# Performance work log

Hardware: AMD Instinct MI355X
Metric: run time of the kernel (lower is better)

Reference implementation:

```python
import jax, jax.numpy as jnp
import numpy as np
from jax import lax

B, C, H, W = 64, 256, 32, 32
EPS = 1e-5


def setup_inputs() -> dict:
    key = jax.random.key(0)
    ks = jax.random.split(key, 11)
    c = C
    return {
        "x": jax.random.normal(ks[0], (B, C, H, W), jnp.float32),
        "bn1_gamma": jax.random.uniform(ks[1], (c,), jnp.float32, 0.5, 1.5),
        "bn1_beta": 0.1 * jax.random.normal(ks[2], (c,), jnp.float32),
        "bn1_mean": 0.1 * jax.random.normal(ks[3], (c,), jnp.float32),
        "bn1_var": jax.random.uniform(ks[4], (c,), jnp.float32, 0.5, 1.5),
        "w1": 0.05 * jax.random.normal(ks[5], (c, c, 3, 3), jnp.float32),
        "bn2_gamma": jax.random.uniform(ks[6], (c,), jnp.float32, 0.5, 1.5),
        "bn2_beta": 0.1 * jax.random.normal(ks[7], (c,), jnp.float32),
        "bn2_mean": 0.1 * jax.random.normal(ks[8], (c,), jnp.float32),
        "bn2_var": jax.random.uniform(ks[9], (c,), jnp.float32, 0.5, 1.5),
        "w2": 0.05 * jax.random.normal(ks[10], (c, c, 3, 3), jnp.float32),
    }


def _bn(x, gamma, beta, mean, var):
    # eval-mode BatchNorm2d over channel axis of NCHW
    inv = gamma * lax.rsqrt(var + EPS)
    return x * inv[None, :, None, None] + (beta - mean * inv)[None, :, None, None]


def _binarize(x):
    # TBN binary activations {-1,+1}, straight-through in bwd
    s = jnp.where(x >= 0, 1.0, -1.0).astype(x.dtype)
    return x + lax.stop_gradient(s - x)


def _ternarize(w):
    # TBN ternary weights alpha*{-1,0,+1}; delta = 0.7*mean|W|
    aw = jnp.abs(w)
    delta = 0.7 * jnp.mean(aw)
    mask = (aw > delta).astype(w.dtype)
    alpha = jnp.sum(aw * mask) / jnp.maximum(jnp.sum(mask), 1.0)
    wq = alpha * jnp.sign(w) * mask
    return w + lax.stop_gradient(wq - w)


def _tbn_conv3x3(x, w, stride):
    return lax.conv_general_dilated(
        _binarize(x), _ternarize(w),
        window_strides=(stride, stride), padding=[(1, 1), (1, 1)],
        dimension_numbers=("NCHW", "OIHW", "NCHW"))


def reference(x, bn1_gamma, bn1_beta, bn1_mean, bn1_var, w1,
              bn2_gamma, bn2_beta, bn2_mean, bn2_var, w2):
    identity = x
    h = _tbn_conv3x3(_bn(x, bn1_gamma, bn1_beta, bn1_mean, bn1_var), w1, 1)
    h = _tbn_conv3x3(_bn(h, bn2_gamma, bn2_beta, bn2_mean, bn2_var), w2, 1)
    return identity + h  # ShortCut downsample
```

## Files before the change

### kernel.cpp

```cpp
#include <hip/hip_runtime.h>
#include <stdint.h>


#define EPS 1e-5f

typedef int i32x4  __attribute__((ext_vector_type(4)));
typedef int i32x16 __attribute__((ext_vector_type(16)));

__device__ __forceinline__ void gload16(const void* g, void* l) {
  __builtin_amdgcn_global_load_lds(
      (const __attribute__((address_space(1))) void*)g,
      (__attribute__((address_space(3))) void*)l, 16, 0, 0);
}

__global__ __launch_bounds__(256) void wsum_kernel(const float* __restrict__ w,
                                                   float* __restrict__ partial) {
  __shared__ float red[256];
  const int t = threadIdx.x;
  const int b = blockIdx.x;
  float s = 0.f;
#pragma unroll
  for (int i = 0; i < 32; ++i) s += fabsf(w[b * 256 + t + i * 18432]);
  red[t] = s;
  __syncthreads();
  for (int o = 128; o > 0; o >>= 1) {
    if (t < o) red[t] += red[t + o];
    __syncthreads();
  }
  if (t == 0) partial[b] = red[0];
}

__global__ void delta_kernel(const float* __restrict__ p1, const float* __restrict__ p2,
                             float* __restrict__ delta) {
  const int t = threadIdx.x;
  if (t < 2) {
    const float* p = (t == 0) ? p1 : p2;
    double s = 0.0;
    for (int i = 0; i < 72; ++i) s += (double)p[i];
    delta[t] = 0.7f * (float)(s * (1.0 / 589824.0));
  }
}

__global__ __launch_bounds__(256) void quant_kernel(const float* __restrict__ w,
                                                    const float* __restrict__ delta2, const int didx,
                                                    int8_t* __restrict__ wq,
                                                    float* __restrict__ psum,
                                                    float* __restrict__ pcnt) {
  __shared__ float rs[256];
  __shared__ float rc[256];
  const int t = threadIdx.x;
  const int idx = blockIdx.x * 256 + t;
  const float d = delta2[didx];
  const float v = w[idx];
  const float av = fabsf(v);
  const bool m = av > d;
  const int co = idx / 2304;
  const int rem = idx - co * 2304;
  const int ci = rem / 9;
  const int tap = rem - ci * 9;
  wq[(co >> 5) * 73728 + (ci >> 6) * 18432 + tap * 2048 +
     (((ci & 63) >> 4) << 9) + ((co & 31) << 4) + (ci & 15)] =
      m ? (v > 0.f ? (int8_t)1 : (int8_t)-1) : (int8_t)0;
  rs[t] = m ? av : 0.f;
  rc[t] = m ? 1.f : 0.f;
  __syncthreads();
  for (int o = 128; o > 0; o >>= 1) {
    if (t < o) { rs[t] += rs[t + o]; rc[t] += rc[t + o]; }
    __syncthreads();
  }
  if (t == 0) { psum[blockIdx.x] = rs[0]; pcnt[blockIdx.x] = rc[0]; }
}

__global__ __launch_bounds__(256) void alpha_kernel(const float* __restrict__ ps1, const float* __restrict__ pc1,
                                                    const float* __restrict__ ps2, const float* __restrict__ pc2,
                                                    const float* __restrict__ g2, const float* __restrict__ b2,
                                                    const float* __restrict__ m2, const float* __restrict__ v2,
                                                    float* __restrict__ alphas,
                                                    float* __restrict__ inv2o, float* __restrict__ add2o) {
  __shared__ float rs[256];
  __shared__ float rc[256];
  const int t = threadIdx.x;
  float s1 = 0.f, c1 = 0.f, s2 = 0.f, c2 = 0.f;
#pragma unroll
  for (int i = 0; i < 9; ++i) {
    s1 += ps1[t + (i << 8)]; c1 += pc1[t + (i << 8)];
    s2 += ps2[t + (i << 8)]; c2 += pc2[t + (i << 8)];
  }
  rs[t] = s1; rc[t] = c1;
  __syncthreads();
  for (int o = 128; o > 0; o >>= 1) {
    if (t < o) { rs[t] += rs[t + o]; rc[t] += rc[t + o]; }
    __syncthreads();
  }
  if (t == 0) alphas[0] = rs[0] / fmaxf(rc[0], 1.f);
  __syncthreads();
  rs[t] = s2; rc[t] = c2;
  __syncthreads();
  for (int o = 128; o > 0; o >>= 1) {
    if (t < o) { rs[t] += rs[t + o]; rc[t] += rc[t + o]; }
    __syncthreads();
  }
  if (t == 0) alphas[1] = rs[0] / fmaxf(rc[0], 1.f);
  const float inv = g2[t] * rsqrtf(v2[t] + EPS);
  inv2o[t] = inv;
  add2o[t] = b2[t] - m2[t] * inv;
}

__global__ __launch_bounds__(256) void bn_bin_kernel(const float* __restrict__ x,
                                                     const float* __restrict__ g1,
                                                     const float* __restrict__ b1,
                                                     const float* __restrict__ m1,
                                                     const float* __restrict__ v1,
                                                     int8_t* __restrict__ a1) {
  __shared__ int8_t lds[64 * 40];
  const int t = threadIdx.x;
  const int p0 = blockIdx.x << 6;
  const int c0 = blockIdx.y << 5;
  const int n = blockIdx.z;
  const int pl = t & 63;
  const int cl0 = t >> 6;
#pragma unroll
  for (int i = 0; i < 8; ++i) {
    const int cl = cl0 + (i << 2);
    const int c = c0 + cl;
    const float inv = g1[c] * rsqrtf(v1[c] + EPS);
    const float ad = b1[c] - m1[c] * inv;
    const float val = x[(((n << 8) + c) << 10) + p0 + pl];
    const float tt = fmaf(val, inv, ad);
    lds[pl * 40 + cl] = (tt >= 0.f) ? (int8_t)1 : (int8_t)-1;
  }
  __syncthreads();
  const int pl2 = t >> 2;
  const int s2 = (t & 3) << 3;
  const uint2 o = *(const uint2*)&lds[pl2 * 40 + s2];
  *(uint2*)&a1[(((n << 10) + p0 + pl2) << 8) + c0 + s2] = o;
}

template <int EPI>
__global__ __launch_bounds__(256, 4) void conv3x3_tbn(
    const int8_t* __restrict__ act,
    const int8_t* __restrict__ wq,
    const float* __restrict__ alphas, const int aidx,
    const float* __restrict__ inv2, const float* __restrict__ add2,
    const float* __restrict__ xres,
    int8_t* __restrict__ aout, float* __restrict__ fout) {
  __shared__ int8_t ldsA[4 * 321 * 16];
  __shared__ int8_t ldsB[9 * 4 * 32 * 16];

  const int tid = threadIdx.x;
  const int bid = blockIdx.x;
  const int L = (bid & 7) * 256 + (bid >> 3);
  const int mb = L >> 3;
  const int nb = L & 7;
  const int n = mb >> 2;
  const int y0 = (mb & 3) << 3;
  const int l = tid & 63;
  const int wid = tid >> 6;
  const int lx = l & 31;
  const int lh = l >> 5;

  int srcA[5], dstA[5];
#pragma unroll
  for (int i = 0; i < 5; ++i) {
    const int idx = tid + (i << 8);
    const int asl = idx / 320;
    const int apx = idx - asl * 320;
    int ys = y0 - 1 + (apx >> 5);
    ys = ys < 0 ? 0 : (ys > 31 ? 31 : ys);
    srcA[i] = (((n << 10) + (ys << 5) + (apx & 31)) << 8) + (asl << 4);
    dstA[i] = asl * 5136 + (apx << 4);
  }
  if (tid < 4) *(i32x4*)(ldsA + tid * 5136 + 5120) = (i32x4){0, 0, 0, 0};

  i32x16 acc[2];
  acc[0] = (i32x16)(0);
  acc[1] = (i32x16)(0);

  const int8_t* wbase = wq + nb * 73728;

#pragma unroll
  for (int i = 0; i < 5; ++i) gload16(act + srcA[i], ldsA + dstA[i]);
#pragma unroll
  for (int i = 0; i < 4; ++i)
    gload16(wbase + ((tid + (i << 8)) << 4), ldsB + ((tid + (i << 8)) << 4));
  if (tid < 128) gload16(wbase + ((tid + 1024) << 4), ldsB + ((tid + 1024) << 4));
  __syncthreads();

  for (int chunk = 0; chunk < 4; ++chunk) {
    __builtin_amdgcn_s_setprio(1);
#pragma unroll
    for (int tap = 0; tap < 9; ++tap) {
      const int ky = tap / 3, kx = tap % 3;
      const int xs = lx + kx - 1;
      const bool xok = (unsigned)xs < 32u;
      int apix[2];
#pragma unroll
      for (int mt = 0; mt < 2; ++mt) {
        const int yr = (wid << 1) + mt + ky;
        const bool ok = xok && ((unsigned)(y0 - 1 + yr) < 32u);
        apix[mt] = ok ? (yr << 5) + xs : 320;
      }
      i32x4 bfr[2], afr[2][2];
#pragma unroll
      for (int kh = 0; kh < 2; ++kh) {
        const int sl = lh + (kh << 1);
        bfr[kh] = *(const i32x4*)(ldsB + (tap << 11) + (sl << 9) + (lx << 4));
#pragma unroll
        for (int mt = 0; mt < 2; ++mt)
          afr[mt][kh] = *(const i32x4*)(ldsA + sl * 5136 + (apix[mt] << 4));
      }
#pragma unroll
      for (int mt = 0; mt < 2; ++mt)
#pragma unroll
        for (int kh = 0; kh < 2; ++kh)
          acc[mt] = __builtin_amdgcn_mfma_i32_32x32x32_i8(afr[mt][kh], bfr[kh], acc[mt], 0, 0, 0);
    }
    __builtin_amdgcn_s_setprio(0);
    if (chunk < 3) {
      __syncthreads();
#pragma unroll
      for (int i = 0; i < 5; ++i)
        gload16(act + srcA[i] + ((chunk + 1) << 6), ldsA + dstA[i]);
      const int8_t* wch = wbase + (chunk + 1) * 18432;
#pragma unroll
      for (int i = 0; i < 4; ++i)
        gload16(wch + ((tid + (i << 8)) << 4), ldsB + ((tid + (i << 8)) << 4));
      if (tid < 128) gload16(wch + ((tid + 1024) << 4), ldsB + ((tid + 1024) << 4));
      __syncthreads();
    }
  }

  const float alpha = alphas[aidx];
  const int co = (nb << 5) + lx;
  if constexpr (EPI == 0) {
    const float inv = inv2[co];
    const float ad = add2[co];
#pragma unroll
    for (int mt = 0; mt < 2; ++mt) {
      const int pixbase = (mb << 8) + (((wid << 1) + mt) << 5) + (lh << 2);
#pragma unroll
      for (int rg = 0; rg < 16; ++rg) {
        const int pix = pixbase + (rg & 3) + ((rg >> 2) << 3);
        const float h = alpha * (float)acc[mt][rg];
        const float tt = fmaf(h, inv, ad);
        aout[(pix << 8) + co] = (tt >= 0.f) ? (int8_t)1 : (int8_t)-1;
      }
    }
  } else {
#pragma unroll
    for (int mt = 0; mt < 2; ++mt) {
      const int pimg0 = ((mb & 3) << 8) + (((wid << 1) + mt) << 5) + (lh << 2);
#pragma unroll
      for (int qd = 0; qd < 4; ++qd) {
        const int off = (((n << 8) + co) << 10) + pimg0 + (qd << 3);
        const float4 xv = *(const float4*)(xres + off);
        float4 o;
        o.x = xv.x + alpha * (float)acc[mt][qd * 4 + 0];
        o.y = xv.y + alpha * (float)acc[mt][qd * 4 + 1];
        o.z = xv.z + alpha * (float)acc[mt][qd * 4 + 2];
        o.w = xv.w + alpha * (float)acc[mt][qd * 4 + 3];
        *(float4*)(fout + off) = o;
      }
    }
  }
}

extern "C" void kernel_launch(void* const* d_in, const int* in_sizes, int n_in,
                              void* d_out, int out_size, void* d_ws, size_t ws_size,
                              hipStream_t stream) {
  const float* x  = (const float*)d_in[0];
  const float* g1 = (const float*)d_in[1];
  const float* b1 = (const float*)d_in[2];
  const float* m1 = (const float*)d_in[3];
  const float* v1 = (const float*)d_in[4];
  const float* w1 = (const float*)d_in[5];
  const float* g2 = (const float*)d_in[6];
  const float* b2 = (const float*)d_in[7];
  const float* m2 = (const float*)d_in[8];
  const float* v2 = (const float*)d_in[9];
  const float* w2 = (const float*)d_in[10];
  float* out = (float*)d_out;

  char* ws = (char*)d_ws;
  int8_t* a1  = (int8_t*)(ws);
  int8_t* a2  = (int8_t*)(ws + 16777216);
  int8_t* wq1 = (int8_t*)(ws + 33554432);
  int8_t* wq2 = (int8_t*)(ws + 33554432 + 589824);
  float* fs = (float*)(ws + 33554432 + 1179648);
  float* pd1    = fs;
  float* pd2    = fs + 128;
  float* deltas = fs + 256;
  float* alphas = fs + 260;
  float* ps1    = fs + 512;
  float* pc1    = fs + 512 + 2304;
  float* ps2    = fs + 512 + 4608;
  float* pc2    = fs + 512 + 6912;
  float* inv2   = fs + 512 + 9216;
  float* add2   = fs + 512 + 9472;

  hipLaunchKernelGGL(wsum_kernel, dim3(72), dim3(256), 0, stream, w1, pd1);
  hipLaunchKernelGGL(wsum_kernel, dim3(72), dim3(256), 0, stream, w2, pd2);
  hipLaunchKernelGGL(delta_kernel, dim3(1), dim3(64), 0, stream, pd1, pd2, deltas);
  hipLaunchKernelGGL(quant_kernel, dim3(2304), dim3(256), 0, stream, w1, deltas, 0, wq1, ps1, pc1);
  hipLaunchKernelGGL(quant_kernel, dim3(2304), dim3(256), 0, stream, w2, deltas, 1, wq2, ps2, pc2);
  hipLaunchKernelGGL(alpha_kernel, dim3(1), dim3(256), 0, stream,
                     ps1, pc1, ps2, pc2, g2, b2, m2, v2, alphas, inv2, add2);
  hipLaunchKernelGGL(bn_bin_kernel, dim3(16, 8, 64), dim3(256), 0, stream, x, g1, b1, m1, v1, a1);
  hipLaunchKernelGGL((conv3x3_tbn<0>), dim3(2048), dim3(256), 0, stream,
                     a1, wq1, alphas, 0, inv2, add2, (const float*)nullptr,
                     a2, (float*)nullptr);
  hipLaunchKernelGGL((conv3x3_tbn<1>), dim3(2048), dim3(256), 0, stream,
                     a2, wq2, alphas, 1, (const float*)nullptr, (const float*)nullptr, x,
                     (int8_t*)nullptr, out);
  (void)in_sizes; (void)n_in; (void)out_size; (void)ws_size;
}
```

Baseline: 135.7 us.

## Enlarge conv tile to 16 rows x 64 channels with 512-thread blocks

The int8 MFMA conv kernel now uses 512-thread blocks. Each block covers 16 output rows by 64 output channels instead of 8 rows by 32 channels, and each wave holds a 2x2 grid of 32x32 accumulators. The weight quantization layout is changed to match 64-channel groups. This is meant to improve reuse of activation and weight fragments loaded from LDS and global memory, and to reduce halo overhead. In exchange it uses more LDS and registers per block and launches fewer blocks (512), which may reduce occupancy.

```diff
diff --git a/kernel.cpp b/kernel.cpp
--- a/kernel.cpp
+++ b/kernel.cpp
@@ -58,8 +58,8 @@
   const int rem = idx - co * 2304;
   const int ci = rem / 9;
   const int tap = rem - ci * 9;
-  wq[(co >> 5) * 73728 + (ci >> 6) * 18432 + tap * 2048 +
-     (((ci & 63) >> 4) << 9) + ((co & 31) << 4) + (ci & 15)] =
+  wq[(co >> 6) * 147456 + (ci >> 6) * 36864 + tap * 4096 +
+     (((ci & 63) >> 4) << 10) + ((co & 63) << 4) + (ci & 15)] =
       m ? (v > 0.f ? (int8_t)1 : (int8_t)-1) : (int8_t)0;
   rs[t] = m ? av : 0.f;
   rc[t] = m ? 1.f : 0.f;
@@ -137,53 +137,56 @@
 }
 
 template <int EPI>
-__global__ __launch_bounds__(256, 4) void conv3x3_tbn(
+__global__ __launch_bounds__(512, 4) void conv3x3_tbn(
     const int8_t* __restrict__ act,
     const int8_t* __restrict__ wq,
     const float* __restrict__ alphas, const int aidx,
     const float* __restrict__ inv2, const float* __restrict__ add2,
     const float* __restrict__ xres,
     int8_t* __restrict__ aout, float* __restrict__ fout) {
-  __shared__ int8_t ldsA[4 * 321 * 16];
-  __shared__ int8_t ldsB[9 * 4 * 32 * 16];
+  __shared__ int8_t ldsA[4 * 577 * 16];
+  __shared__ int8_t ldsB[9 * 4 * 64 * 16];
 
   const int tid = threadIdx.x;
   const int bid = blockIdx.x;
-  const int L = (bid & 7) * 256 + (bid >> 3);
-  const int mb = L >> 3;
-  const int nb = L & 7;
-  const int n = mb >> 2;
-  const int y0 = (mb & 3) << 3;
+  const int L = (bid & 7) * 64 + (bid >> 3);
+  const int mb = L >> 2;
+  const int nb = L & 3;
+  const int n = mb >> 1;
+  const int y0 = (mb & 1) << 4;
   const int l = tid & 63;
   const int wid = tid >> 6;
   const int lx = l & 31;
   const int lh = l >> 5;
 
-  int srcA[5], dstA[5];
+  int srcA[5];
 #pragma unroll
   for (int i = 0; i < 5; ++i) {
-    const int idx = tid + (i << 8);
-    const int asl = idx / 320;
-    const int apx = idx - asl * 320;
+    const int idx = tid + (i << 9);
+    const int asl = idx / 576;
+    const int apx = idx - asl * 576;
     int ys = y0 - 1 + (apx >> 5);
     ys = ys < 0 ? 0 : (ys > 31 ? 31 : ys);
     srcA[i] = (((n << 10) + (ys << 5) + (apx & 31)) << 8) + (asl << 4);
-    dstA[i] = asl * 5136 + (apx << 4);
-  }
-  if (tid < 4) *(i32x4*)(ldsA + tid * 5136 + 5120) = (i32x4){0, 0, 0, 0};
-
-  i32x16 acc[2];
-  acc[0] = (i32x16)(0);
-  acc[1] = (i32x16)(0);
-
-  const int8_t* wbase = wq + nb * 73728;
-
-#pragma unroll
-  for (int i = 0; i < 5; ++i) gload16(act + srcA[i], ldsA + dstA[i]);
-#pragma unroll
-  for (int i = 0; i < 4; ++i)
-    gload16(wbase + ((tid + (i << 8)) << 4), ldsB + ((tid + (i << 8)) << 4));
-  if (tid < 128) gload16(wbase + ((tid + 1024) << 4), ldsB + ((tid + 1024) << 4));
+  }
+  if (tid < 4) *(i32x4*)(ldsA + tid * 9232 + 9216) = (i32x4){0, 0, 0, 0};
+
+  i32x16 acc[2][2];
+  acc[0][0] = (i32x16)(0); acc[0][1] = (i32x16)(0);
+  acc[1][0] = (i32x16)(0); acc[1][1] = (i32x16)(0);
+
+  const int8_t* wbase = wq + nb * 147456;
+
+#pragma unroll
+  for (int i = 0; i < 5; ++i) {
+    const int idx = tid + (i << 9);
+    if (i < 4 || tid < 256) {
+      const int asl = idx / 576;
+      const int apx = idx - asl * 576;
+      gload16(act + srcA[i], ldsA + asl * 9232 + (apx << 4));
+      gload16(wbase + (idx << 4), ldsB + (idx << 4));
+    }
+  }
   __syncthreads();
 
   for (int chunk = 0; chunk < 4; ++chunk) {
@@ -198,68 +201,82 @@
       for (int mt = 0; mt < 2; ++mt) {
         const int yr = (wid << 1) + mt + ky;
         const bool ok = xok && ((unsigned)(y0 - 1 + yr) < 32u);
-        apix[mt] = ok ? (yr << 5) + xs : 320;
-      }
-      i32x4 bfr[2], afr[2][2];
+        apix[mt] = ok ? (yr << 5) + xs : 576;
+      }
+      i32x4 afr[2][2], bfr[2][2];
 #pragma unroll
       for (int kh = 0; kh < 2; ++kh) {
         const int sl = lh + (kh << 1);
-        bfr[kh] = *(const i32x4*)(ldsB + (tap << 11) + (sl << 9) + (lx << 4));
 #pragma unroll
         for (int mt = 0; mt < 2; ++mt)
-          afr[mt][kh] = *(const i32x4*)(ldsA + sl * 5136 + (apix[mt] << 4));
+          afr[mt][kh] = *(const i32x4*)(ldsA + sl * 9232 + (apix[mt] << 4));
+#pragma unroll
+        for (int nt = 0; nt < 2; ++nt)
+          bfr[nt][kh] = *(const i32x4*)(ldsB + (tap << 12) + (sl << 10) + ((nt << 5) + lx) * 16);
       }
 #pragma unroll
       for (int mt = 0; mt < 2; ++mt)
 #pragma unroll
-        for (int kh = 0; kh < 2; ++kh)
-          acc[mt] = __builtin_amdgcn_mfma_i32_32x32x32_i8(afr[mt][kh], bfr[kh], acc[mt], 0, 0, 0);
+        for (int nt = 0; nt < 2; ++nt)
+#pragma unroll
+          for (int kh = 0; kh < 2; ++kh)
+            acc[mt][nt] = __builtin_amdgcn_mfma_i32_32x32x32_i8(afr[mt][kh], bfr[nt][kh], acc[mt][nt], 0, 0, 0);
     }
     __builtin_amdgcn_s_setprio(0);
     if (chunk < 3) {
       __syncthreads();
-#pragma unroll
-      for (int i = 0; i < 5; ++i)
-        gload16(act + srcA[i] + ((chunk + 1) << 6), ldsA + dstA[i]);
-      const int8_t* wch = wbase + (chunk + 1) * 18432;
-#pragma unroll
-      for (int i = 0; i < 4; ++i)
-        gload16(wch + ((tid + (i << 8)) << 4), ldsB + ((tid + (i << 8)) << 4));
-      if (tid < 128) gload16(wch + ((tid + 1024) << 4), ldsB + ((tid + 1024) << 4));
+      const int8_t* wch = wbase + (chunk + 1) * 36864;
+#pragma unroll
+      for (int i = 0; i < 5; ++i) {
+        const int idx = tid + (i << 9);
+        if (i < 4 || tid < 256) {
+          const int asl = idx / 576;
+          const int apx = idx - asl * 576;
+          gload16(act + srcA[i] + ((chunk + 1) << 6), ldsA + asl * 9232 + (apx << 4));
+          gload16(wch + (idx << 4), ldsB + (idx << 4));
+        }
+      }
       __syncthreads();
     }
   }
 
   const float alpha = alphas[aidx];
-  const int co = (nb << 5) + lx;
   if constexpr (EPI == 0) {
-    const float inv = inv2[co];
-    const float ad = add2[co];
-#pragma unroll
-    for (int mt = 0; mt < 2; ++mt) {
-      const int pixbase = (mb << 8) + (((wid << 1) + mt) << 5) + (lh << 2);
-#pragma unroll
-      for (int rg = 0; rg < 16; ++rg) {
-        const int pix = pixbase + (rg & 3) + ((rg >> 2) << 3);
-        const float h = alpha * (float)acc[mt][rg];
-        const float tt = fmaf(h, inv, ad);
-        aout[(pix << 8) + co] = (tt >= 0.f) ? (int8_t)1 : (int8_t)-1;
+#pragma unroll
+    for (int nt = 0; nt < 2; ++nt) {
+      const int co = (nb << 6) + (nt << 5) + lx;
+      const float inv = inv2[co];
+      const float ad = add2[co];
+#pragma unroll
+      for (int mt = 0; mt < 2; ++mt) {
+        const int pixbase = (mb << 9) + (((wid << 1) + mt) << 5) + (lh << 2);
+#pragma unroll
+        for (int rg = 0; rg < 16; ++rg) {
+          const int pix = pixbase + (rg & 3) + ((rg >> 2) << 3);
+          const float h = alpha * (float)acc[mt][nt][rg];
+          const float tt = fmaf(h, inv, ad);
+          aout[(pix << 8) + co] = (tt >= 0.f) ? (int8_t)1 : (int8_t)-1;
+        }
       }
     }
   } else {
 #pragma unroll
-    for (int mt = 0; mt < 2; ++mt) {
-      const int pimg0 = ((mb & 3) << 8) + (((wid << 1) + mt) << 5) + (lh << 2);
-#pragma unroll
-      for (int qd = 0; qd < 4; ++qd) {
-        const int off = (((n << 8) + co) << 10) + pimg0 + (qd << 3);
-        const float4 xv = *(const float4*)(xres + off);
-        float4 o;
-        o.x = xv.x + alpha * (float)acc[mt][qd * 4 + 0];
-        o.y = xv.y + alpha * (float)acc[mt][qd * 4 + 1];
-        o.z = xv.z + alpha * (float)acc[mt][qd * 4 + 2];
-        o.w = xv.w + alpha * (float)acc[mt][qd * 4 + 3];
-        *(float4*)(fout + off) = o;
+    for (int nt = 0; nt < 2; ++nt) {
+      const int co = (nb << 6) + (nt << 5) + lx;
+#pragma unroll
+      for (int mt = 0; mt < 2; ++mt) {
+        const int pimg0 = ((mb & 1) << 9) + (((wid << 1) + mt) << 5) + (lh << 2);
+#pragma unroll
+        for (int qd = 0; qd < 4; ++qd) {
+          const int off = (((n << 8) + co) << 10) + pimg0 + (qd << 3);
+          const float4 xv = *(const float4*)(xres + off);
+          float4 o;
+          o.x = xv.x + alpha * (float)acc[mt][nt][qd * 4 + 0];
+          o.y = xv.y + alpha * (float)acc[mt][nt][qd * 4 + 1];
+          o.z = xv.z + alpha * (float)acc[mt][nt][qd * 4 + 2];
+          o.w = xv.w + alpha * (float)acc[mt][nt][qd * 4 + 3];
+          *(float4*)(fout + off) = o;
+        }
       }
     }
   }
@@ -306,10 +323,10 @@
   hipLaunchKernelGGL(alpha_kernel, dim3(1), dim3(256), 0, stream,
                      ps1, pc1, ps2, pc2, g2, b2, m2, v2, alphas, inv2, add2);
   hipLaunchKernelGGL(bn_bin_kernel, dim3(16, 8, 64), dim3(256), 0, stream, x, g1, b1, m1, v1, a1);
-  hipLaunchKernelGGL((conv3x3_tbn<0>), dim3(2048), dim3(256), 0, stream,
+  hipLaunchKernelGGL((conv3x3_tbn<0>), dim3(512), dim3(512), 0, stream,
                      a1, wq1, alphas, 0, inv2, add2, (const float*)nullptr,
                      a2, (float*)nullptr);
-  hipLaunchKernelGGL((conv3x3_tbn<1>), dim3(2048), dim3(256), 0, stream,
+  hipLaunchKernelGGL((conv3x3_tbn<1>), dim3(512), dim3(512), 0, stream,
                      a2, wq2, alphas, 1, (const float*)nullptr, (const float*)nullptr, x,
                      (int8_t*)nullptr, out);
   (void)in_sizes; (void)n_in; (void)out_size; (void)ws_size;
```

Result: faster. 132.3 us (-2.5%).

## Double-buffer conv LDS with larger 512x64 tiles and merge weight-prep launches

Applied to the files above, without the earlier changes.

The conv kernel moves to 512-thread blocks, each computing 16 output rows by 64 output channels with four accumulators per wave. K-chunks shrink to 32 input channels and are double-buffered in LDS, so the next chunk's global-to-LDS loads are issued before the current chunk's MFMAs, with register-level fragment ping-pong between taps. This should improve data reuse and overlap memory with compute, at the cost of more LDS per block (about 78 KB) and lower occupancy. Separately, the wsum and quant launches for the two weight tensors are merged into single 2D-grid launches, and the weight layout is reorganised to match the new tiling.

```diff
diff --git a/kernel.cpp b/kernel.cpp
--- a/kernel.cpp
+++ b/kernel.cpp
@@ -13,11 +13,13 @@
       (__attribute__((address_space(3))) void*)l, 16, 0, 0);
 }
 
-__global__ __launch_bounds__(256) void wsum_kernel(const float* __restrict__ w,
+__global__ __launch_bounds__(256) void wsum_kernel(const float* __restrict__ w1,
+                                                   const float* __restrict__ w2,
                                                    float* __restrict__ partial) {
   __shared__ float red[256];
   const int t = threadIdx.x;
   const int b = blockIdx.x;
+  const float* w = blockIdx.y ? w2 : w1;
   float s = 0.f;
 #pragma unroll
   for (int i = 0; i < 32; ++i) s += fabsf(w[b * 256 + t + i * 18432]);
@@ -27,7 +29,7 @@
     if (t < o) red[t] += red[t + o];
     __syncthreads();
   }
-  if (t == 0) partial[b] = red[0];
+  if (t == 0) partial[(blockIdx.y << 7) + b] = red[0];
 }
 
 __global__ void delta_kernel(const float* __restrict__ p1, const float* __restrict__ p2,
@@ -41,16 +43,20 @@
   }
 }
 
-__global__ __launch_bounds__(256) void quant_kernel(const float* __restrict__ w,
-                                                    const float* __restrict__ delta2, const int didx,
-                                                    int8_t* __restrict__ wq,
-                                                    float* __restrict__ psum,
-                                                    float* __restrict__ pcnt) {
+__global__ __launch_bounds__(256) void quant_kernel(const float* __restrict__ w1,
+                                                    const float* __restrict__ w2,
+                                                    const float* __restrict__ delta2,
+                                                    int8_t* __restrict__ wq1,
+                                                    int8_t* __restrict__ wq2,
+                                                    float* __restrict__ psbase) {
   __shared__ float rs[256];
   __shared__ float rc[256];
   const int t = threadIdx.x;
+  const int by = blockIdx.y;
+  const float* w = by ? w2 : w1;
+  int8_t* wq = by ? wq2 : wq1;
   const int idx = blockIdx.x * 256 + t;
-  const float d = delta2[didx];
+  const float d = delta2[by];
   const float v = w[idx];
   const float av = fabsf(v);
   const bool m = av > d;
@@ -58,8 +64,8 @@
   const int rem = idx - co * 2304;
   const int ci = rem / 9;
   const int tap = rem - ci * 9;
-  wq[(co >> 5) * 73728 + (ci >> 6) * 18432 + tap * 2048 +
-     (((ci & 63) >> 4) << 9) + ((co & 31) << 4) + (ci & 15)] =
+  wq[(co >> 6) * 147456 + (ci >> 5) * 18432 + tap * 2048 +
+     (((ci & 31) >> 4) << 10) + ((co & 63) << 4) + (ci & 15)] =
       m ? (v > 0.f ? (int8_t)1 : (int8_t)-1) : (int8_t)0;
   rs[t] = m ? av : 0.f;
   rc[t] = m ? 1.f : 0.f;
@@ -68,7 +74,8 @@
     if (t < o) { rs[t] += rs[t + o]; rc[t] += rc[t + o]; }
     __syncthreads();
   }
-  if (t == 0) { psum[blockIdx.x] = rs[0]; pcnt[blockIdx.x] = rc[0]; }
+  if (t == 0) { psbase[by * 4608 + blockIdx.x] = rs[0];
+                psbase[by * 4608 + 2304 + blockIdx.x] = rc[0]; }
 }
 
 __global__ __launch_bounds__(256) void alpha_kernel(const float* __restrict__ ps1, const float* __restrict__ pc1,
@@ -136,132 +143,166 @@
   *(uint2*)&a1[(((n << 10) + p0 + pl2) << 8) + c0 + s2] = o;
 }
 
+struct Frag { i32x4 a0, a1, b0, b1; };
+
+#define LOADF(F, TAP, AR, BR) do {                                          \
+  F.a0 = *(const i32x4*)((AR) + aOff0[TAP]);                                \
+  F.a1 = *(const i32x4*)((AR) + aOff1[TAP]);                                \
+  F.b0 = *(const i32x4*)((BR) + bOff + (TAP) * 2048);                       \
+  F.b1 = *(const i32x4*)((BR) + bOff + (TAP) * 2048 + 512);                 \
+} while (0)
+
+#define MMAF(F) do {                                                        \
+  __builtin_amdgcn_s_setprio(1);                                            \
+  acc00 = __builtin_amdgcn_mfma_i32_32x32x32_i8(F.a0, F.b0, acc00, 0, 0, 0);\
+  acc01 = __builtin_amdgcn_mfma_i32_32x32x32_i8(F.a0, F.b1, acc01, 0, 0, 0);\
+  acc10 = __builtin_amdgcn_mfma_i32_32x32x32_i8(F.a1, F.b0, acc10, 0, 0, 0);\
+  acc11 = __builtin_amdgcn_mfma_i32_32x32x32_i8(F.a1, F.b1, acc11, 0, 0, 0);\
+  __builtin_amdgcn_s_setprio(0);                                            \
+} while (0)
+
+#define STAGE(CH, AW, BW) do {                                              \
+  const int8_t* wch = wnb + (CH) * 18432;                                   \
+  _Pragma("unroll")                                                         \
+  for (int i = 0; i < 5; ++i) {                                             \
+    if (i < 4 || tid < 256) {                                               \
+      if (stA[i]) gload16(act + sOff[i] + ((CH) << 5), (AW) + dOff[i]);     \
+      else        gload16(wch + sOff[i], (BW) + dOff[i]);                   \
+    }                                                                       \
+  }                                                                         \
+} while (0)
+
+#define CHUNK(CH, AR, BR, AW, BW, DOSTAGE) do {                             \
+  if (DOSTAGE) STAGE((CH) + 1, AW, BW);                                     \
+  Frag fa, fb;                                                              \
+  LOADF(fa, 0, AR, BR); LOADF(fb, 1, AR, BR);                               \
+  MMAF(fa);                                                                 \
+  LOADF(fa, 2, AR, BR); MMAF(fb);                                           \
+  LOADF(fb, 3, AR, BR); MMAF(fa);                                           \
+  LOADF(fa, 4, AR, BR); MMAF(fb);                                           \
+  LOADF(fb, 5, AR, BR); MMAF(fa);                                           \
+  LOADF(fa, 6, AR, BR); MMAF(fb);                                           \
+  LOADF(fb, 7, AR, BR); MMAF(fa);                                           \
+  LOADF(fa, 8, AR, BR); MMAF(fb);                                           \
+  MMAF(fa);                                                                 \
+} while (0)
+
 template <int EPI>
-__global__ __launch_bounds__(256, 4) void conv3x3_tbn(
+__global__ __launch_bounds__(512, 2) void conv3x3_tbn(
     const int8_t* __restrict__ act,
     const int8_t* __restrict__ wq,
     const float* __restrict__ alphas, const int aidx,
     const float* __restrict__ inv2, const float* __restrict__ add2,
     const float* __restrict__ xres,
     int8_t* __restrict__ aout, float* __restrict__ fout) {
-  __shared__ int8_t ldsA[4 * 321 * 16];
-  __shared__ int8_t ldsB[9 * 4 * 32 * 16];
+  __shared__ int8_t ldsA0[2 * 577 * 16];
+  __shared__ int8_t ldsA1[2 * 577 * 16];
+  __shared__ int8_t ldsB0[9 * 2 * 64 * 16];
+  __shared__ int8_t ldsB1[9 * 2 * 64 * 16];
 
   const int tid = threadIdx.x;
   const int bid = blockIdx.x;
-  const int L = (bid & 7) * 256 + (bid >> 3);
-  const int mb = L >> 3;
-  const int nb = L & 7;
-  const int n = mb >> 2;
-  const int y0 = (mb & 3) << 3;
+  const int L = (bid & 7) * 64 + (bid >> 3);
+  const int mb = L >> 2;
+  const int nb = L & 3;
+  const int n = mb >> 1;
+  const int y0 = (mb & 1) << 4;
   const int l = tid & 63;
   const int wid = tid >> 6;
   const int lx = l & 31;
   const int lh = l >> 5;
 
-  int srcA[5], dstA[5];
+  int aOff0[9], aOff1[9];
+#pragma unroll
+  for (int tap = 0; tap < 9; ++tap) {
+    const int ky = tap / 3, kx = tap % 3;
+    const int xs = lx + kx - 1;
+    const bool xok = (unsigned)xs < 32u;
+#pragma unroll
+    for (int mt = 0; mt < 2; ++mt) {
+      const int yr = (wid << 1) + mt + ky;
+      const bool ok = xok && ((unsigned)(y0 - 1 + yr) < 32u);
+      const int apix = ok ? (yr << 5) + xs : 576;
+      const int off = lh * 9232 + (apix << 4);
+      if (mt == 0) aOff0[tap] = off; else aOff1[tap] = off;
+    }
+  }
+  const int bOff = (lh << 10) + (lx << 4);
+
+  bool stA[5];
+  int sOff[5], dOff[5];
 #pragma unroll
   for (int i = 0; i < 5; ++i) {
-    const int idx = tid + (i << 8);
-    const int asl = idx / 320;
-    const int apx = idx - asl * 320;
-    int ys = y0 - 1 + (apx >> 5);
-    ys = ys < 0 ? 0 : (ys > 31 ? 31 : ys);
-    srcA[i] = (((n << 10) + (ys << 5) + (apx & 31)) << 8) + (asl << 4);
-    dstA[i] = asl * 5136 + (apx << 4);
-  }
-  if (tid < 4) *(i32x4*)(ldsA + tid * 5136 + 5120) = (i32x4){0, 0, 0, 0};
-
-  i32x16 acc[2];
-  acc[0] = (i32x16)(0);
-  acc[1] = (i32x16)(0);
-
-  const int8_t* wbase = wq + nb * 73728;
-
-#pragma unroll
-  for (int i = 0; i < 5; ++i) gload16(act + srcA[i], ldsA + dstA[i]);
-#pragma unroll
-  for (int i = 0; i < 4; ++i)
-    gload16(wbase + ((tid + (i << 8)) << 4), ldsB + ((tid + (i << 8)) << 4));
-  if (tid < 128) gload16(wbase + ((tid + 1024) << 4), ldsB + ((tid + 1024) << 4));
-  __syncthreads();
-
-  for (int chunk = 0; chunk < 4; ++chunk) {
-    __builtin_amdgcn_s_setprio(1);
-#pragma unroll
-    for (int tap = 0; tap < 9; ++tap) {
-      const int ky = tap / 3, kx = tap % 3;
-      const int xs = lx + kx - 1;
-      const bool xok = (unsigned)xs < 32u;
-      int apix[2];
-#pragma unroll
-      for (int mt = 0; mt < 2; ++mt) {
-        const int yr = (wid << 1) + mt + ky;
-        const bool ok = xok && ((unsigned)(y0 - 1 + yr) < 32u);
-        apix[mt] = ok ? (yr << 5) + xs : 320;
-      }
-      i32x4 bfr[2], afr[2][2];
-#pragma unroll
-      for (int kh = 0; kh < 2; ++kh) {
-        const int sl = lh + (kh << 1);
-        bfr[kh] = *(const i32x4*)(ldsB + (tap << 11) + (sl << 9) + (lx << 4));
-#pragma unroll
-        for (int mt = 0; mt < 2; ++mt)
-          afr[mt][kh] = *(const i32x4*)(ldsA + sl * 5136 + (apix[mt] << 4));
-      }
-#pragma unroll
-      for (int mt = 0; mt < 2; ++mt)
-#pragma unroll
-        for (int kh = 0; kh < 2; ++kh)
-          acc[mt] = __builtin_amdgcn_mfma_i32_32x32x32_i8(afr[mt][kh], bfr[kh], acc[mt], 0, 0, 0);
+    const int idx = tid + (i << 9);
+    if (idx < 1152) {
+      stA[i] = true;
+      const int sl = idx / 576;
+      const int px = idx - sl * 576;
+      int ys = y0 - 1 + (px >> 5);
+      ys = ys < 0 ? 0 : (ys > 31 ? 31 : ys);
+      sOff[i] = (((n << 10) + (ys << 5) + (px & 31)) << 8) + (sl << 4);
+      dOff[i] = sl * 9232 + (px << 4);
+    } else {
+      stA[i] = false;
+      const int j = idx - 1152;
+      sOff[i] = j << 4;
+      dOff[i] = j << 4;
     }
-    __builtin_amdgcn_s_setprio(0);
-    if (chunk < 3) {
-      __syncthreads();
-#pragma unroll
-      for (int i = 0; i < 5; ++i)
-        gload16(act + srcA[i] + ((chunk + 1) << 6), ldsA + dstA[i]);
-      const int8_t* wch = wbase + (chunk + 1) * 18432;
-#pragma unroll
-      for (int i = 0; i < 4; ++i)
-        gload16(wch + ((tid + (i << 8)) << 4), ldsB + ((tid + (i << 8)) << 4));
-      if (tid < 128) gload16(wch + ((tid + 1024) << 4), ldsB + ((tid + 1024) << 4));
-      __syncthreads();
-    }
-  }
+  }
+
+  i32x16 acc00 = (i32x16)(0), acc01 = (i32x16)(0);
+  i32x16 acc10 = (i32x16)(0), acc11 = (i32x16)(0);
+
+  const int8_t* wnb = wq + nb * 147456;
+
+  if (tid < 4) {
+    int8_t* zb = (tid & 2) ? ldsA1 : ldsA0;
+    *(i32x4*)(zb + (tid & 1) * 9232 + 9216) = (i32x4){0, 0, 0, 0};
+  }
+
+  STAGE(0, ldsA0, ldsB0);
+  __syncthreads();
+
+  CHUNK(0, ldsA0, ldsB0, ldsA1, ldsB1, true);  __syncthreads();
+  CHUNK(1, ldsA1, ldsB1, ldsA0, ldsB0, true);  __syncthreads();
+  CHUNK(2, ldsA0, ldsB0, ldsA1, ldsB1, true);  __syncthreads();
+  CHUNK(3, ldsA1, ldsB1, ldsA0, ldsB0, true);  __syncthreads();
+  CHUNK(4, ldsA0, ldsB0, ldsA1, ldsB1, true);  __syncthreads();
+  CHUNK(5, ldsA1, ldsB1, ldsA0, ldsB0, true);  __syncthreads();
+  CHUNK(6, ldsA0, ldsB0, ldsA1, ldsB1, true);  __syncthreads();
+  CHUNK(7, ldsA1, ldsB1, ldsA0, ldsB0, false);
 
   const float alpha = alphas[aidx];
-  const int co = (nb << 5) + lx;
   if constexpr (EPI == 0) {
-    const float inv = inv2[co];
-    const float ad = add2[co];
-#pragma unroll
-    for (int mt = 0; mt < 2; ++mt) {
-      const int pixbase = (mb << 8) + (((wid << 1) + mt) << 5) + (lh << 2);
-#pragma unroll
-      for (int rg = 0; rg < 16; ++rg) {
-        const int pix = pixbase + (rg & 3) + ((rg >> 2) << 3);
-        const float h = alpha * (float)acc[mt][rg];
-        const float tt = fmaf(h, inv, ad);
-        aout[(pix << 8) + co] = (tt >= 0.f) ? (int8_t)1 : (int8_t)-1;
-      }
-    }
+#define EPI0(ACC, MT, NT) {                                                  \
+    const int co = (nb << 6) + ((NT) << 5) + lx;                             \
+    const float inv = inv2[co];                                              \
+    const float ad = add2[co];                                               \
+    const int pixbase = (mb << 9) + (((wid << 1) + (MT)) << 5) + (lh << 2);  \
+    _Pragma("unroll")                                                        \
+    for (int rg = 0; rg < 16; ++rg) {                                        \
+      const int pix = pixbase + (rg & 3) + ((rg >> 2) << 3);                 \
+      const float h = alpha * (float)ACC[rg];                                \
+      const float tt = fmaf(h, inv, ad);                                     \
+      aout[(pix << 8) + co] = (tt >= 0.f) ? (int8_t)1 : (int8_t)-1;          \
+    } }
+    EPI0(acc00, 0, 0); EPI0(acc01, 0, 1); EPI0(acc10, 1, 0); EPI0(acc11, 1, 1);
   } else {
-#pragma unroll
-    for (int mt = 0; mt < 2; ++mt) {
-      const int pimg0 = ((mb & 3) << 8) + (((wid << 1) + mt) << 5) + (lh << 2);
-#pragma unroll
-      for (int qd = 0; qd < 4; ++qd) {
-        const int off = (((n << 8) + co) << 10) + pimg0 + (qd << 3);
-        const float4 xv = *(const float4*)(xres + off);
-        float4 o;
-        o.x = xv.x + alpha * (float)acc[mt][qd * 4 + 0];
-        o.y = xv.y + alpha * (float)acc[mt][qd * 4 + 1];
-        o.z = xv.z + alpha * (float)acc[mt][qd * 4 + 2];
-        o.w = xv.w + alpha * (float)acc[mt][qd * 4 + 3];
-        *(float4*)(fout + off) = o;
-      }
-    }
+#define EPI1(ACC, MT, NT) {                                                  \
+    const int co = (nb << 6) + ((NT) << 5) + lx;                             \
+    const int pimg0 = ((mb & 1) << 9) + (((wid << 1) + (MT)) << 5) + (lh << 2); \
+    _Pragma("unroll")                                                        \
+    for (int qd = 0; qd < 4; ++qd) {                                         \
+      const int off = (((n << 8) + co) << 10) + pimg0 + (qd << 3);           \
+      const float4 xv = *(const float4*)(xres + off);                        \
+      float4 o;                                                              \
+      o.x = xv.x + alpha * (float)ACC[qd * 4 + 0];                           \
+      o.y = xv.y + alpha * (float)ACC[qd * 4 + 1];                           \
+      o.z = xv.z + alpha * (float)ACC[qd * 4 + 2];                           \
+      o.w = xv.w + alpha * (float)ACC[qd * 4 + 3];                           \
+      *(float4*)(fout + off) = o;                                            \
+    } }
+    EPI1(acc00, 0, 0); EPI1(acc01, 0, 1); EPI1(acc10, 1, 0); EPI1(acc11, 1, 1);
   }
 }
 
@@ -291,25 +332,22 @@
   float* pd2    = fs + 128;
   float* deltas = fs + 256;
   float* alphas = fs + 260;
-  float* ps1    = fs + 512;
-  float* pc1    = fs + 512 + 2304;
-  float* ps2    = fs + 512 + 4608;
-  float* pc2    = fs + 512 + 6912;
+  float* psb    = fs + 512;
   float* inv2   = fs + 512 + 9216;
   float* add2   = fs + 512 + 9472;
 
-  hipLaunchKernelGGL(wsum_kernel, dim3(72), dim3(256), 0, stream, w1, pd1);
-  hipLaunchKernelGGL(wsum_kernel, dim3(72), dim3(256), 0, stream, w2, pd2);
+  hipLaunchKernelGGL(wsum_kernel, dim3(72, 2), dim3(256), 0, stream, w1, w2, fs);
   hipLaunchKernelGGL(delta_kernel, dim3(1), dim3(64), 0, stream, pd1, pd2, deltas);
-  hipLaunchKernelGGL(quant_kernel, dim3(2304), dim3(256), 0, stream, w1, deltas, 0, wq1, ps1, pc1);
-  hipLaunchKernelGGL(quant_kernel, dim3(2304), dim3(256), 0, stream, w2, deltas, 1, wq2, ps2, pc2);
+  hipLaunchKernelGGL(quant_kernel, dim3(2304, 2), dim3(256), 0, stream,
+                     w1, w2, deltas, wq1, wq2, psb);
   hipLaunchKernelGGL(alpha_kernel, dim3(1), dim3(256), 0, stream,
-                     ps1, pc1, ps2, pc2, g2, b2, m2, v2, alphas, inv2, add2);
+                     psb, psb + 2304, psb + 4608, psb + 6912,
+                     g2, b2, m2, v2, alphas, inv2, add2);
   hipLaunchKernelGGL(bn_bin_kernel, dim3(16, 8, 64), dim3(256), 0, stream, x, g1, b1, m1, v1, a1);
-  hipLaunchKernelGGL((conv3x3_tbn<0>), dim3(2048), dim3(256), 0, stream,
+  hipLaunchKernelGGL((conv3x3_tbn<0>), dim3(512), dim3(512), 0, stream,
                      a1, wq1, alphas, 0, inv2, add2, (const float*)nullptr,
                      a2, (float*)nullptr);
-  hipLaunchKernelGGL((conv3x3_tbn<1>), dim3(2048), dim3(256), 0, stream,
+  hipLaunchKernelGGL((conv3x3_tbn<1>), dim3(512), dim3(512), 0, stream,
                      a2, wq2, alphas, 1, (const float*)nullptr, (const float*)nullptr, x,
                      (int8_t*)nullptr, out);
   (void)in_sizes; (void)n_in; (void)out_size; (void)ws_size;
```

Result: slower. 283.7 us (+109.1%).
